# Kernel optimization log

Hardware: AMD Instinct MI355X
Metric: run time of the kernel (lower is better)

## Reference

```python
import jax, jax.numpy as jnp
import numpy as np

jax.config.update("jax_enable_x64", True)  # window_sum runs cumsums in double, as in the torch source

WIN = 7
EPS = 0.01


def _gradient(I):
    # forward finite differences, cropping to [D-1, H-1, W-1] (same=False path, reduction='mean')
    c = I[:, :, 1:, 1:, 1:]
    dx = c - I[:, :, :-1, 1:, 1:]
    dy = c - I[:, :, 1:, :-1, 1:]
    dz = c - I[:, :, 1:, 1:, :-1]
    return dx, dy, dz


def _window_sum(I, win):
    # 3D box-filter via triple cumsum on a zero-padded double-precision volume
    if win == 1:
        return I
    half = win // 2
    pad = (half + win % 2, half)
    Ip = jnp.pad(I, ((0, 0), (0, 0), pad, pad, pad)).astype(jnp.float64)
    cs = jnp.cumsum(jnp.cumsum(jnp.cumsum(Ip, axis=2), axis=3), axis=4)
    x, y, z = I.shape[2:]
    w = win
    out = (cs[:, :, w:, w:, w:] - cs[:, :, w:, w:, :z] - cs[:, :, w:, :y, w:]
           - cs[:, :, :x, w:, w:] + cs[:, :, w:, :y, :z] + cs[:, :, :x, w:, :z]
           + cs[:, :, :x, :y, w:] - cs[:, :, :x, :y, :z])
    return out.astype(jnp.float32)


def setup_inputs() -> dict:
    key = jax.random.key(0)
    k1, k2 = jax.random.split(key)
    shape = (2, 1, 160, 192, 160)
    Ii = jax.random.normal(k1, shape, dtype=jnp.float32)
    Ji = jax.random.normal(k2, shape, dtype=jnp.float32)
    return {"Ii": Ii, "Ji": Ji}


def reference(Ii, Ji):
    def det(dx, dy, dz):
        return dx * dx + dy * dy + dz * dz + EPS

    dxI, dyI, dzI = _gradient(Ii)
    dxJ, dyJ, dzJ = _gradient(Ji)
    dx_I = _window_sum(dxI, WIN)
    dy_I = _window_sum(dyI, WIN)
    dz_I = _window_sum(dzI, WIN)
    dx_J = _window_sum(dxJ, WIN)
    dy_J = _window_sum(dyJ, WIN)
    dz_J = _window_sum(dzJ, WIN)
    cross = jnp.abs(dx_I * dx_J + dy_I * dy_J + dz_I * dz_J) + EPS
    norm = jnp.sqrt(det(dx_I, dy_I, dz_I) * det(dx_J, dy_J, dz_J))
    return jnp.mean(cross / norm)
```

## Files before the change

### kernel.cpp

```cpp
#include <hip/hip_runtime.h>

#define IYD 192
#define IZD 160
#define PLANE 30720
#define VOLSZ 4915200
#define YG 191
#define ZG 159

#define RAW_V 660
#define RAW_R 44
#define ZB 1320
#define DB 2400
#define ZD_V 540
#define ZD_R 36
#define TB 3480
#define WB 3992
#define LDSF 4504

#define NVOX_INV (1.0f / 9657342.0f)

__global__ __launch_bounds__(256, 4) void grad_sim_tele(
    const float* __restrict__ Ii, const float* __restrict__ Ji,
    float* __restrict__ out)
{
    __shared__ __align__(16) float lds[LDSF];
    const int tid = threadIdx.x;
    const int z0 = (int)blockIdx.x * 32;
    const int y0 = (int)blockIdx.y * 8;
    const int seg = blockIdx.z & 7;
    const int bat = blockIdx.z >> 3;
    const int s0 = seg * 20;
    const int a0 = (seg == 0) ? 0 : (s0 - 3);
    const int aLast = (seg == 7) ? 159 : (s0 + 23);

    const float* __restrict__ bI = Ii + (size_t)bat * VOLSZ;
    const float* __restrict__ bJ = Ji + (size_t)bat * VOLSZ;

    const float* gp[5];
    int lof[5];
    bool okl[5];
#pragma unroll
    for (int k = 0; k < 5; ++k) {
        int idx = tid + 256 * k;
        bool inr = idx < 1170;
        int id2 = inr ? idx : 0;
        int v = id2 / 585;
        int r = id2 - v * 585;
        int yy = r / 39;
        int zz = r - yy * 39;
        int iy = y0 - 3 + yy;
        int iz = z0 - 3 + zz;
        okl[k] = inr && ((unsigned)iy < IYD) && ((unsigned)iz < IZD);
        int iyc = min(max(iy, 0), IYD - 1);
        int izc = min(max(iz, 0), IZD - 1);
        gp[k] = (v ? bJ : bI) + (iyc * IZD + izc);
        lof[k] = inr ? (v * RAW_V + yy * RAW_R + zz) : 43;
    }

    const int zv = tid / 60;
    const int zrr = tid - 60 * zv;
    const int zr = zrr >> 2;
    const int zq = zrr & 3;
    const bool doZ = tid < 120;
    const bool zlo = (z0 == 0) && (zq == 0);
    const bool zhi = (z0 == 128) && (zq == 3);
    const int rawRd = zv * RAW_V + zr * RAW_R + 8 * zq;
    const int zdWr = zv * ZD_V + zr * ZD_R + 8 * zq;

    const bool doY = tid < 128;
    const int yf = tid >> 5;
    const int yv = yf & 1;
    const int yisW = yf >> 1;
    const int ybase = (yisW ? DB : ZB) + yv * ZD_V + (tid & 31);
    const int yout = (yisW ? WB : TB) + yv * 256 + (tid & 31);

    const int oy = tid >> 5;
    const int oz = tid & 31;
    const int ygl = y0 + oy;
    const int vmax = min(3, 190 - ygl);
    const int vmin = max(-3, -ygl);
    const int relHi = oy + vmax + 4;
    const int relLo = oy + vmin + 3;
    const int vHiI = ZB + relHi * ZD_R + oz;
    const int vLoI = ZB + relLo * ZD_R + oz;
    const bool okyz = (ygl < YG) && ((z0 + oz) < ZG);

    float Tr[2][8], Vr[2][8], Wr[2][8], Sdy[2], Sdz[2];
#pragma unroll
    for (int v = 0; v < 2; ++v) {
#pragma unroll
        for (int j = 0; j < 8; ++j) { Tr[v][j] = 0.f; Vr[v][j] = 0.f; Wr[v][j] = 0.f; }
        Sdy[v] = 0.f; Sdz[v] = 0.f;
    }
    float acc = 0.f;

    {
        const int pb = a0 * PLANE;
        float t[5];
#pragma unroll
        for (int k = 0; k < 5; ++k) t[k] = gp[k][pb];
#pragma unroll
        for (int k = 0; k < 5; ++k) lds[lof[k]] = okl[k] ? t[k] : 0.f;
    }
    __syncthreads();

    for (int ag = (a0 & ~7); ag <= aLast; ag += 8) {
#pragma unroll
        for (int p = 0; p < 8; ++p) {
            const int a = ag + p;
            if (a < a0 || a > aLast) continue;

            const bool dof = (a + 1) <= aLast;
            float pf[5];
            if (dof) {
                const int pb = (a + 1) * PLANE;
#pragma unroll
                for (int k = 0; k < 5; ++k) pf[k] = gp[k][pb];
            }
            if (doZ) {
                float C[16];
                const float4* rb = (const float4*)&lds[rawRd];
#pragma unroll
                for (int u = 0; u < 4; ++u) ((float4*)C)[u] = rb[u];
                float D[8];
#pragma unroll
                for (int i = 0; i < 8; ++i) D[i] = C[i + 7] - C[i];
                if (zlo) { D[0] = C[7] - C[3]; D[1] = C[8] - C[3]; D[2] = C[9] - C[3]; }
                if (zhi) { D[4] = C[10] - C[4]; D[5] = C[10] - C[5];
                           D[6] = C[10] - C[6]; D[7] = C[10] - C[7]; }
                if (zlo) { C[1] = 0.f; C[2] = 0.f; C[3] = 0.f; }
                if (zhi) { C[11] = 0.f; C[12] = 0.f; C[13] = 0.f; C[14] = 0.f; }
                float Z[8];
                float w = C[1] + C[2] + C[3] + C[4] + C[5] + C[6] + C[7];
                Z[0] = w;
#pragma unroll
                for (int m = 1; m < 8; ++m) { w += C[m + 7] - C[m]; Z[m] = w; }
                float4* zb = (float4*)&lds[ZB + zdWr];
                zb[0] = make_float4(Z[0], Z[1], Z[2], Z[3]);
                zb[1] = make_float4(Z[4], Z[5], Z[6], Z[7]);
                float4* db = (float4*)&lds[DB + zdWr];
                db[0] = make_float4(D[0], D[1], D[2], D[3]);
                db[1] = make_float4(D[4], D[5], D[6], D[7]);
            }
            __syncthreads();

            if (doY) {
                float h[15];
#pragma unroll
                for (int r = 1; r < 15; ++r) h[r] = lds[ybase + r * ZD_R];
                if (y0 == 0)   { h[1] = 0.f; h[2] = 0.f; h[3] = 0.f; }
                if (y0 == 184) { h[11] = 0.f; h[12] = 0.f; h[13] = 0.f; h[14] = 0.f; }
                float w = h[1] + h[2] + h[3] + h[4] + h[5] + h[6] + h[7];
                lds[yout] = w;
#pragma unroll
                for (int q = 1; q < 8; ++q) {
                    w += h[q + 7] - h[q];
                    lds[yout + q * 32] = w;
                }
            }
            __syncthreads();

            {
                float tI = lds[TB + tid];
                float tJ = lds[TB + 256 + tid];
                float wI = lds[WB + tid];
                float wJ = lds[WB + 256 + tid];
                float vI = lds[vHiI] - lds[vLoI];
                float vJ = lds[vHiI + ZD_V] - lds[vLoI + ZD_V];
                if (a == a0) { vI = 0.f; vJ = 0.f; wI = 0.f; wJ = 0.f; }
                const int p1 = (p + 1) & 7;
                float hdxI = tI - Tr[0][p1];
                float hdxJ = tJ - Tr[1][p1];
                Sdy[0] += vI - Vr[0][p1]; Vr[0][p] = vI;
                Sdy[1] += vJ - Vr[1][p1]; Vr[1][p] = vJ;
                Sdz[0] += wI - Wr[0][p1]; Wr[0][p] = wI;
                Sdz[1] += wJ - Wr[1][p1]; Wr[1][p] = wJ;
                Tr[0][p] = tI; Tr[1][p] = tJ;
                if (p == 0) {
                    if (a == 0) {
                        Tr[0][5] = tI; Tr[0][6] = tI; Tr[0][7] = tI;
                        Tr[1][5] = tJ; Tr[1][6] = tJ; Tr[1][7] = tJ;
                    }
                }
                if (a >= s0 + 4) {
                    float cross = fabsf(hdxI * hdxJ + Sdy[0] * Sdy[1] + Sdz[0] * Sdz[1]) + 0.01f;
                    float dI = hdxI * hdxI + Sdy[0] * Sdy[0] + Sdz[0] * Sdz[0] + 0.01f;
                    float dJ = hdxJ * hdxJ + Sdy[1] * Sdy[1] + Sdz[1] * Sdz[1] + 0.01f;
                    float val = cross * rsqrtf(dI * dJ);
                    if (okyz) acc += val;
                }
            }
            if (dof) {
#pragma unroll
                for (int k = 0; k < 5; ++k) lds[lof[k]] = okl[k] ? pf[k] : 0.f;
            }
            __syncthreads();
        }
    }

    if (seg == 7) {
#pragma unroll
        for (int t = 0; t < 3; ++t) {
            const int sl = t + 1;
            float hdxI = Tr[0][7] - Tr[0][sl];
            float hdxJ = Tr[1][7] - Tr[1][sl];
            Sdy[0] -= Vr[0][sl]; Sdy[1] -= Vr[1][sl];
            Sdz[0] -= Wr[0][sl]; Sdz[1] -= Wr[1][sl];
            float cross = fabsf(hdxI * hdxJ + Sdy[0] * Sdy[1] + Sdz[0] * Sdz[1]) + 0.01f;
            float dI = hdxI * hdxI + Sdy[0] * Sdy[0] + Sdz[0] * Sdz[0] + 0.01f;
            float dJ = hdxJ * hdxJ + Sdy[1] * Sdy[1] + Sdz[1] * Sdz[1] + 0.01f;
            float val = cross * rsqrtf(dI * dJ);
            if (okyz) acc += val;
        }
    }

#pragma unroll
    for (int off = 32; off > 0; off >>= 1) acc += __shfl_down(acc, off, 64);
    __syncthreads();
    if ((tid & 63) == 0) lds[tid >> 6] = acc;
    __syncthreads();
    if (tid == 0)
        atomicAdd(out, (lds[0] + lds[1] + lds[2] + lds[3]) * NVOX_INV);
}

extern "C" void kernel_launch(void* const* d_in, const int* in_sizes, int n_in,
                              void* d_out, int out_size, void* d_ws, size_t ws_size,
                              hipStream_t stream) {
    const float* Ii = (const float*)d_in[0];
    const float* Ji = (const float*)d_in[1];
    float* out = (float*)d_out;
    hipMemsetAsync(d_out, 0, sizeof(float) * (out_size > 0 ? out_size : 1), stream);
    dim3 grid(5, 24, 16);
    grad_sim_tele<<<grid, dim3(256), 0, stream>>>(Ii, Ji, out);
}
```

Before: 86.21 us.

## Software-pipeline z/y/x stages across planes with double-buffered LDS, one barrier per plane

The per-plane z-pass, y-pass and final x-accumulate stages are skewed across consecutive planes, so each stage works on a different plane in the same iteration. LDS buffers are double-buffered by parity, which cuts the barriers per plane from three to one. The dy window difference is also precomputed by the otherwise idle upper 128 threads into a new LDS buffer. LDS use roughly doubles to about 40KB, which may lower occupancy below the four blocks per CU requested, and two extra drain iterations are added per segment.

```diff
diff --git a/kernel.cpp b/kernel.cpp
--- a/kernel.cpp
+++ b/kernel.cpp
@@ -7,19 +7,23 @@
 #define YG 191
 #define ZG 159
 
-#define RAW_V 660
-#define RAW_R 44
-#define ZB 1320
-#define DB 2400
-#define ZD_V 540
-#define ZD_R 36
-#define TB 3480
-#define WB 3992
-#define LDSF 4504
+#define RAWP 1320
+#define RAWV 660
+#define RAWR 44
+#define ZBB 2640
+#define DBB 4800
+#define ZDP 1080
+#define ZDV 540
+#define ZDR 36
+#define TBB 6960
+#define WBB 7984
+#define VBB 9008
+#define SOP 512
+#define LDSF 10032
 
 #define NVOX_INV (1.0f / 9657342.0f)
 
-__global__ __launch_bounds__(256, 4) void grad_sim_tele(
+__global__ __launch_bounds__(256, 4) void grad_sim_pipe(
     const float* __restrict__ Ii, const float* __restrict__ Ji,
     float* __restrict__ out)
 {
@@ -32,6 +36,7 @@
     const int s0 = seg * 20;
     const int a0 = (seg == 0) ? 0 : (s0 - 3);
     const int aLast = (seg == 7) ? 159 : (s0 + 23);
+    const int tEnd = aLast + 2;
 
     const float* __restrict__ bI = Ii + (size_t)bat * VOLSZ;
     const float* __restrict__ bJ = Ji + (size_t)bat * VOLSZ;
@@ -54,7 +59,7 @@
         int iyc = min(max(iy, 0), IYD - 1);
         int izc = min(max(iz, 0), IZD - 1);
         gp[k] = (v ? bJ : bI) + (iyc * IZD + izc);
-        lof[k] = inr ? (v * RAW_V + yy * RAW_R + zz) : 43;
+        lof[k] = inr ? (v * RAWV + yy * RAWR + zz) : 43;
     }
 
     const int zv = tid / 60;
@@ -64,26 +69,33 @@
     const bool doZ = tid < 120;
     const bool zlo = (z0 == 0) && (zq == 0);
     const bool zhi = (z0 == 128) && (zq == 3);
-    const int rawRd = zv * RAW_V + zr * RAW_R + 8 * zq;
-    const int zdWr = zv * ZD_V + zr * ZD_R + 8 * zq;
-
-    const bool doY = tid < 128;
+    const int rawRd = zv * RAWV + zr * RAWR + 8 * zq;
+    const int zdWr = zv * ZDV + zr * ZDR + 8 * zq;
+
     const int yf = tid >> 5;
     const int yv = yf & 1;
     const int yisW = yf >> 1;
-    const int ybase = (yisW ? DB : ZB) + yv * ZD_V + (tid & 31);
-    const int yout = (yisW ? WB : TB) + yv * 256 + (tid & 31);
+    const int ybase0 = (yisW ? DBB : ZBB) + yv * ZDV + (tid & 31);
+    const int yout0 = (yisW ? WBB : TBB) + yv * 256 + (tid & 31);
+
+    const int qv = (tid - 128) & 127;
+    const int voz = qv & 31;
+    const int vvv = (qv >> 6) & 1;
+    const int oyb = (qv >> 5) & 1;
+    int rH36[4], rL36[4], vbo[4];
+#pragma unroll
+    for (int k = 0; k < 4; ++k) {
+        int oyk = oyb + 2 * k;
+        int ygl = y0 + oyk;
+        rH36[k] = (oyk + min(3, 190 - ygl) + 4) * ZDR;
+        rL36[k] = (oyk + max(-3, -ygl) + 3) * ZDR;
+        vbo[k] = vvv * 256 + oyk * 32 + voz;
+    }
+    const int zb2base = vvv * ZDV + voz;
 
     const int oy = tid >> 5;
     const int oz = tid & 31;
-    const int ygl = y0 + oy;
-    const int vmax = min(3, 190 - ygl);
-    const int vmin = max(-3, -ygl);
-    const int relHi = oy + vmax + 4;
-    const int relLo = oy + vmin + 3;
-    const int vHiI = ZB + relHi * ZD_R + oz;
-    const int vLoI = ZB + relLo * ZD_R + oz;
-    const bool okyz = (ygl < YG) && ((z0 + oz) < ZG);
+    const bool okyz = ((y0 + oy) < YG) && ((z0 + oz) < ZG);
 
     float Tr[2][8], Vr[2][8], Wr[2][8], Sdy[2], Sdz[2];
 #pragma unroll
@@ -96,32 +108,37 @@
 
     {
         const int pb = a0 * PLANE;
+        const int po = (a0 & 1) * RAWP;
         float t[5];
 #pragma unroll
         for (int k = 0; k < 5; ++k) t[k] = gp[k][pb];
 #pragma unroll
-        for (int k = 0; k < 5; ++k) lds[lof[k]] = okl[k] ? t[k] : 0.f;
+        for (int k = 0; k < 5; ++k) lds[po + lof[k]] = okl[k] ? t[k] : 0.f;
     }
     __syncthreads();
 
-    for (int ag = (a0 & ~7); ag <= aLast; ag += 8) {
-#pragma unroll
-        for (int p = 0; p < 8; ++p) {
-            const int a = ag + p;
-            if (a < a0 || a > aLast) continue;
-
-            const bool dof = (a + 1) <= aLast;
+    for (int ag = (a0 & ~7); ag <= tEnd; ag += 8) {
+#pragma unroll
+        for (int u = 0; u < 8; ++u) {
+            const int t = ag + u;
+            if (t < a0 || t > tEnd) continue;
+
+            const int par1 = u & 1;
+            const int par2 = (u + 1) & 1;
+
+            const bool dof = (t + 1) <= aLast;
             float pf[5];
             if (dof) {
-                const int pb = (a + 1) * PLANE;
+                const int pb = (t + 1) * PLANE;
 #pragma unroll
                 for (int k = 0; k < 5; ++k) pf[k] = gp[k][pb];
             }
-            if (doZ) {
+
+            if (t <= aLast && doZ) {
                 float C[16];
-                const float4* rb = (const float4*)&lds[rawRd];
-#pragma unroll
-                for (int u = 0; u < 4; ++u) ((float4*)C)[u] = rb[u];
+                const float4* rb = (const float4*)&lds[par1 * RAWP + rawRd];
+#pragma unroll
+                for (int q = 0; q < 4; ++q) ((float4*)C)[q] = rb[q];
                 float D[8];
 #pragma unroll
                 for (int i = 0; i < 8; ++i) D[i] = C[i + 7] - C[i];
@@ -135,39 +152,53 @@
                 Z[0] = w;
 #pragma unroll
                 for (int m = 1; m < 8; ++m) { w += C[m + 7] - C[m]; Z[m] = w; }
-                float4* zb = (float4*)&lds[ZB + zdWr];
+                float4* zb = (float4*)&lds[ZBB + par1 * ZDP + zdWr];
                 zb[0] = make_float4(Z[0], Z[1], Z[2], Z[3]);
                 zb[1] = make_float4(Z[4], Z[5], Z[6], Z[7]);
-                float4* db = (float4*)&lds[DB + zdWr];
+                float4* db = (float4*)&lds[DBB + par1 * ZDP + zdWr];
                 db[0] = make_float4(D[0], D[1], D[2], D[3]);
                 db[1] = make_float4(D[4], D[5], D[6], D[7]);
             }
-            __syncthreads();
-
-            if (doY) {
-                float h[15];
-#pragma unroll
-                for (int r = 1; r < 15; ++r) h[r] = lds[ybase + r * ZD_R];
-                if (y0 == 0)   { h[1] = 0.f; h[2] = 0.f; h[3] = 0.f; }
-                if (y0 == 184) { h[11] = 0.f; h[12] = 0.f; h[13] = 0.f; h[14] = 0.f; }
-                float w = h[1] + h[2] + h[3] + h[4] + h[5] + h[6] + h[7];
-                lds[yout] = w;
-#pragma unroll
-                for (int q = 1; q < 8; ++q) {
-                    w += h[q + 7] - h[q];
-                    lds[yout + q * 32] = w;
+
+            if (t - 1 >= a0 && t - 1 <= aLast) {
+                if (tid < 128) {
+                    const int ybase = ybase0 + par2 * ZDP;
+                    const int yout = yout0 + par2 * SOP;
+                    float h[15];
+#pragma unroll
+                    for (int r = 1; r < 15; ++r) h[r] = lds[ybase + r * ZDR];
+                    if (y0 == 0)   { h[1] = 0.f; h[2] = 0.f; h[3] = 0.f; }
+                    if (y0 == 184) { h[11] = 0.f; h[12] = 0.f; h[13] = 0.f; h[14] = 0.f; }
+                    float w = h[1] + h[2] + h[3] + h[4] + h[5] + h[6] + h[7];
+                    lds[yout] = w;
+#pragma unroll
+                    for (int q = 1; q < 8; ++q) {
+                        w += h[q + 7] - h[q];
+                        lds[yout + q * 32] = w;
+                    }
+                } else {
+                    const int zb2 = ZBB + par2 * ZDP + zb2base;
+                    const int vout = VBB + par2 * SOP;
+#pragma unroll
+                    for (int k = 0; k < 4; ++k) {
+                        float hi = lds[zb2 + rH36[k]];
+                        float lo = lds[zb2 + rL36[k]];
+                        lds[vout + vbo[k]] = hi - lo;
+                    }
                 }
             }
-            __syncthreads();
-
-            {
-                float tI = lds[TB + tid];
-                float tJ = lds[TB + 256 + tid];
-                float wI = lds[WB + tid];
-                float wJ = lds[WB + 256 + tid];
-                float vI = lds[vHiI] - lds[vLoI];
-                float vJ = lds[vHiI + ZD_V] - lds[vLoI + ZD_V];
+
+            if (t - 2 >= a0) {
+                const int a = t - 2;
+                const int sb = par1 * SOP;
+                float tI = lds[TBB + sb + tid];
+                float tJ = lds[TBB + sb + 256 + tid];
+                float wI = lds[WBB + sb + tid];
+                float wJ = lds[WBB + sb + 256 + tid];
+                float vI = lds[VBB + sb + tid];
+                float vJ = lds[VBB + sb + 256 + tid];
                 if (a == a0) { vI = 0.f; vJ = 0.f; wI = 0.f; wJ = 0.f; }
+                const int p = (u + 6) & 7;
                 const int p1 = (p + 1) & 7;
                 float hdxI = tI - Tr[0][p1];
                 float hdxJ = tJ - Tr[1][p1];
@@ -176,11 +207,9 @@
                 Sdz[0] += wI - Wr[0][p1]; Wr[0][p] = wI;
                 Sdz[1] += wJ - Wr[1][p1]; Wr[1][p] = wJ;
                 Tr[0][p] = tI; Tr[1][p] = tJ;
-                if (p == 0) {
-                    if (a == 0) {
-                        Tr[0][5] = tI; Tr[0][6] = tI; Tr[0][7] = tI;
-                        Tr[1][5] = tJ; Tr[1][6] = tJ; Tr[1][7] = tJ;
-                    }
+                if (p == 0 && a == 0) {
+                    Tr[0][5] = tI; Tr[0][6] = tI; Tr[0][7] = tI;
+                    Tr[1][5] = tJ; Tr[1][6] = tJ; Tr[1][7] = tJ;
                 }
                 if (a >= s0 + 4) {
                     float cross = fabsf(hdxI * hdxJ + Sdy[0] * Sdy[1] + Sdz[0] * Sdz[1]) + 0.01f;
@@ -190,9 +219,11 @@
                     if (okyz) acc += val;
                 }
             }
+
             if (dof) {
-#pragma unroll
-                for (int k = 0; k < 5; ++k) lds[lof[k]] = okl[k] ? pf[k] : 0.f;
+                const int po = ((u + 1) & 1) * RAWP;
+#pragma unroll
+                for (int k = 0; k < 5; ++k) lds[po + lof[k]] = okl[k] ? pf[k] : 0.f;
             }
             __syncthreads();
         }
@@ -200,8 +231,8 @@
 
     if (seg == 7) {
 #pragma unroll
-        for (int t = 0; t < 3; ++t) {
-            const int sl = t + 1;
+        for (int tt = 0; tt < 3; ++tt) {
+            const int sl = tt + 1;
             float hdxI = Tr[0][7] - Tr[0][sl];
             float hdxJ = Tr[1][7] - Tr[1][sl];
             Sdy[0] -= Vr[0][sl]; Sdy[1] -= Vr[1][sl];
@@ -231,5 +262,5 @@
     float* out = (float*)d_out;
     hipMemsetAsync(d_out, 0, sizeof(float) * (out_size > 0 ? out_size : 1), stream);
     dim3 grid(5, 24, 16);
-    grad_sim_tele<<<grid, dim3(256), 0, stream>>>(Ii, Ji, out);
+    grad_sim_pipe<<<grid, dim3(256), 0, stream>>>(Ii, Ji, out);
 }
```

Measured after the change: 90.87 us. 5.4% more time.

## Vectorize plane loads to float4, widen Y-pass, halve depth segments

Applied to the files above, without the earlier changes.

Each input plane tile is now loaded as float4 chunks aligned to 4-element z boundaries, replacing scalar gathers. The raw LDS layout shifts by one element to suit this. The Y-direction box sum now runs on 64 threads, each handling a float4 of z and half of the y outputs. The x-axis is split into 4 segments of 40 instead of 8 of 20, which cuts halo recomputation but halves the grid to 960 blocks, lowering parallelism. Out-of-range chunks are zeroed by multiplying with a mask, which assumes the clamped loads hold finite values.

```diff
diff --git a/kernel.cpp b/kernel.cpp
--- a/kernel.cpp
+++ b/kernel.cpp
@@ -7,19 +7,19 @@
 #define YG 191
 #define ZG 159
 
-#define RAW_V 660
-#define RAW_R 44
-#define ZB 1320
-#define DB 2400
-#define ZD_V 540
-#define ZD_R 36
-#define TB 3480
-#define WB 3992
-#define LDSF 4504
+#define RAWV 660
+#define RAWR 44
+#define ZBB 1324
+#define DBB 2404
+#define ZDV 540
+#define ZDR 36
+#define TBB 3484
+#define WBB 3996
+#define LDSF 4508
 
 #define NVOX_INV (1.0f / 9657342.0f)
 
-__global__ __launch_bounds__(256, 4) void grad_sim_tele(
+__global__ __launch_bounds__(256, 4) void grad_sim_v7(
     const float* __restrict__ Ii, const float* __restrict__ Ji,
     float* __restrict__ out)
 {
@@ -27,34 +27,48 @@
     const int tid = threadIdx.x;
     const int z0 = (int)blockIdx.x * 32;
     const int y0 = (int)blockIdx.y * 8;
-    const int seg = blockIdx.z & 7;
-    const int bat = blockIdx.z >> 3;
-    const int s0 = seg * 20;
+    const int seg = blockIdx.z & 3;
+    const int bat = blockIdx.z >> 2;
+    const int s0 = seg * 40;
     const int a0 = (seg == 0) ? 0 : (s0 - 3);
-    const int aLast = (seg == 7) ? 159 : (s0 + 23);
+    const int aLast = (seg == 3) ? 159 : (s0 + 43);
 
     const float* __restrict__ bI = Ii + (size_t)bat * VOLSZ;
     const float* __restrict__ bJ = Ji + (size_t)bat * VOLSZ;
 
-    const float* gp[5];
-    int lof[5];
-    bool okl[5];
-#pragma unroll
-    for (int k = 0; k < 5; ++k) {
-        int idx = tid + 256 * k;
-        bool inr = idx < 1170;
-        int id2 = inr ? idx : 0;
-        int v = id2 / 585;
-        int r = id2 - v * 585;
-        int yy = r / 39;
-        int zz = r - yy * 39;
-        int iy = y0 - 3 + yy;
-        int iz = z0 - 3 + zz;
-        okl[k] = inr && ((unsigned)iy < IYD) && ((unsigned)iz < IZD);
+    const float* gq0;
+    const float* gq1;
+    int lq0, lq1;
+    float mq0, mq1;
+    {
+        int q = tid;
+        int v = q / 150;
+        int rr = q - v * 150;
+        int row = rr / 10;
+        int qd = rr - row * 10;
+        int iy = y0 - 3 + row;
+        int izb = z0 - 4 + 4 * qd;
+        bool ok = ((unsigned)iy < IYD) && (izb >= 0) && (izb + 3 <= 159);
         int iyc = min(max(iy, 0), IYD - 1);
-        int izc = min(max(iz, 0), IZD - 1);
-        gp[k] = (v ? bJ : bI) + (iyc * IZD + izc);
-        lof[k] = inr ? (v * RAW_V + yy * RAW_R + zz) : 43;
+        int izc = min(max(izb, 0), 156);
+        gq0 = (v ? bJ : bI) + (iyc * IZD + izc);
+        lq0 = v * RAWV + row * RAWR + 4 * qd;
+        mq0 = ok ? 1.f : 0.f;
+    }
+    {
+        int q = 256 + tid;
+        int v = q / 150;
+        int rr = q - v * 150;
+        int row = rr / 10;
+        int qd = rr - row * 10;
+        int iy = y0 - 3 + row;
+        int izb = z0 - 4 + 4 * qd;
+        bool ok = ((unsigned)iy < IYD) && (izb >= 0) && (izb + 3 <= 159);
+        int iyc = min(max(iy, 0), IYD - 1);
+        int izc = min(max(izb, 0), 156);
+        gq1 = (v ? bJ : bI) + (iyc * IZD + izc);
+        lq1 = v * RAWV + row * RAWR + 4 * qd;
+        mq1 = ok ? 1.f : 0.f;
     }
 
     const int zv = tid / 60;
@@ -64,25 +78,27 @@
     const bool doZ = tid < 120;
     const bool zlo = (z0 == 0) && (zq == 0);
     const bool zhi = (z0 == 128) && (zq == 3);
-    const int rawRd = zv * RAW_V + zr * RAW_R + 8 * zq;
-    const int zdWr = zv * ZD_V + zr * ZD_R + 8 * zq;
-
-    const bool doY = tid < 128;
-    const int yf = tid >> 5;
-    const int yv = yf & 1;
-    const int yisW = yf >> 1;
-    const int ybase = (yisW ? DB : ZB) + yv * ZD_V + (tid & 31);
-    const int yout = (yisW ? WB : TB) + yv * 256 + (tid & 31);
+    const int rawRd = zv * RAWV + zr * RAWR + 8 * zq;
+    const int zdWr = zv * ZDV + zr * ZDR + 8 * zq;
+
+    const int e2half = tid & 1;
+    const int e2c = tid >> 1;
+    const int e2zq = e2c & 7;
+    const int e2f = (e2c >> 3) & 1;
+    const int e2v = e2c >> 4;
+    const bool doY = tid < 64;
+    const int e2base = (e2f ? DBB : ZBB) + e2v * ZDV + 4 * e2zq;
+    const int e2out = (e2f ? WBB : TBB) + e2v * 256 + 4 * e2zq;
+    const float mlo = (y0 == 0) ? 0.f : 1.f;
+    const float mhi = (y0 == 184) ? 0.f : 1.f;
 
     const int oy = tid >> 5;
     const int oz = tid & 31;
     const int ygl = y0 + oy;
     const int vmax = min(3, 190 - ygl);
     const int vmin = max(-3, -ygl);
-    const int relHi = oy + vmax + 4;
-    const int relLo = oy + vmin + 3;
-    const int vHiI = ZB + relHi * ZD_R + oz;
-    const int vLoI = ZB + relLo * ZD_R + oz;
+    const int vHiI = ZBB + (oy + vmax + 4) * ZDR + oz;
+    const int vLoI = ZBB + (oy + vmin + 3) * ZDR + oz;
     const bool okyz = (ygl < YG) && ((z0 + oz) < ZG);
 
     float Tr[2][8], Vr[2][8], Wr[2][8], Sdy[2], Sdz[2];
@@ -95,80 +111,116 @@
     float acc = 0.f;
 
     {
-        const int pb = a0 * PLANE;
-        float t[5];
-#pragma unroll
-        for (int k = 0; k < 5; ++k) t[k] = gp[k][pb];
-#pragma unroll
-        for (int k = 0; k < 5; ++k) lds[lof[k]] = okl[k] ? t[k] : 0.f;
+        const size_t pb = (size_t)a0 * PLANE;
+        float4 t0 = *(const float4*)(gq0 + pb);
+        t0.x *= mq0; t0.y *= mq0; t0.z *= mq0; t0.w *= mq0;
+        *(float4*)&lds[lq0] = t0;
+        if (tid < 44) {
+            float4 t1 = *(const float4*)(gq1 + pb);
+            t1.x *= mq1; t1.y *= mq1; t1.z *= mq1; t1.w *= mq1;
+            *(float4*)&lds[lq1] = t1;
+        }
     }
     __syncthreads();
 
     for (int ag = (a0 & ~7); ag <= aLast; ag += 8) {
 #pragma unroll
-        for (int p = 0; p < 8; ++p) {
-            const int a = ag + p;
+        for (int u = 0; u < 8; ++u) {
+            const int a = ag + u;
             if (a < a0 || a > aLast) continue;
 
             const bool dof = (a + 1) <= aLast;
-            float pf[5];
+            float4 pf0, pf1;
             if (dof) {
-                const int pb = (a + 1) * PLANE;
-#pragma unroll
-                for (int k = 0; k < 5; ++k) pf[k] = gp[k][pb];
-            }
+                const size_t pb = (size_t)(a + 1) * PLANE;
+                pf0 = *(const float4*)(gq0 + pb);
+                if (tid < 44) pf1 = *(const float4*)(gq1 + pb);
+            }
+
             if (doZ) {
                 float C[16];
                 const float4* rb = (const float4*)&lds[rawRd];
 #pragma unroll
-                for (int u = 0; u < 4; ++u) ((float4*)C)[u] = rb[u];
+                for (int q = 0; q < 4; ++q) ((float4*)C)[q] = rb[q];
                 float D[8];
 #pragma unroll
-                for (int i = 0; i < 8; ++i) D[i] = C[i + 7] - C[i];
-                if (zlo) { D[0] = C[7] - C[3]; D[1] = C[8] - C[3]; D[2] = C[9] - C[3]; }
-                if (zhi) { D[4] = C[10] - C[4]; D[5] = C[10] - C[5];
-                           D[6] = C[10] - C[6]; D[7] = C[10] - C[7]; }
-                if (zlo) { C[1] = 0.f; C[2] = 0.f; C[3] = 0.f; }
-                if (zhi) { C[11] = 0.f; C[12] = 0.f; C[13] = 0.f; C[14] = 0.f; }
+                for (int i = 0; i < 8; ++i) D[i] = C[i + 8] - C[i + 1];
+                if (zlo) { D[0] = C[8] - C[4]; D[1] = C[9] - C[4]; D[2] = C[10] - C[4]; }
+                if (zhi) { D[4] = C[11] - C[5]; D[5] = C[11] - C[6];
+                           D[6] = C[11] - C[7]; D[7] = C[11] - C[8]; }
+                if (zlo) { C[2] = 0.f; C[3] = 0.f; C[4] = 0.f; }
                 float Z[8];
-                float w = C[1] + C[2] + C[3] + C[4] + C[5] + C[6] + C[7];
+                float w = C[2] + C[3] + C[4] + C[5] + C[6] + C[7] + C[8];
                 Z[0] = w;
 #pragma unroll
-                for (int m = 1; m < 8; ++m) { w += C[m + 7] - C[m]; Z[m] = w; }
-                float4* zb = (float4*)&lds[ZB + zdWr];
+                for (int m = 1; m < 8; ++m) { w += C[m + 8] - C[m + 1]; Z[m] = w; }
+                float4* zb = (float4*)&lds[ZBB + zdWr];
                 zb[0] = make_float4(Z[0], Z[1], Z[2], Z[3]);
                 zb[1] = make_float4(Z[4], Z[5], Z[6], Z[7]);
-                float4* db = (float4*)&lds[DB + zdWr];
+                float4* db = (float4*)&lds[DBB + zdWr];
                 db[0] = make_float4(D[0], D[1], D[2], D[3]);
                 db[1] = make_float4(D[4], D[5], D[6], D[7]);
             }
             __syncthreads();
 
             if (doY) {
-                float h[15];
-#pragma unroll
-                for (int r = 1; r < 15; ++r) h[r] = lds[ybase + r * ZD_R];
-                if (y0 == 0)   { h[1] = 0.f; h[2] = 0.f; h[3] = 0.f; }
-                if (y0 == 184) { h[11] = 0.f; h[12] = 0.f; h[13] = 0.f; h[14] = 0.f; }
-                float w = h[1] + h[2] + h[3] + h[4] + h[5] + h[6] + h[7];
-                lds[yout] = w;
-#pragma unroll
-                for (int q = 1; q < 8; ++q) {
-                    w += h[q + 7] - h[q];
-                    lds[yout + q * 32] = w;
+                float4 r[11];
+                const int r0 = e2half ? 4 : 1;
+#pragma unroll
+                for (int i = 0; i < 11; ++i)
+                    r[i] = *(const float4*)&lds[e2base + (r0 + i) * ZDR];
+                if (e2half == 0) {
+                    r[0].x *= mlo; r[0].y *= mlo; r[0].z *= mlo; r[0].w *= mlo;
+                    r[1].x *= mlo; r[1].y *= mlo; r[1].z *= mlo; r[1].w *= mlo;
+                    r[2].x *= mlo; r[2].y *= mlo; r[2].z *= mlo; r[2].w *= mlo;
+                    r[10].x *= mhi; r[10].y *= mhi; r[10].z *= mhi; r[10].w *= mhi;
+                    float4 w;
+                    w.x = r[0].x + r[1].x + r[2].x + r[3].x + r[4].x + r[5].x + r[6].x;
+                    w.y = r[0].y + r[1].y + r[2].y + r[3].y + r[4].y + r[5].y + r[6].y;
+                    w.z = r[0].z + r[1].z + r[2].z + r[3].z + r[4].z + r[5].z + r[6].z;
+                    w.w = r[0].w + r[1].w + r[2].w + r[3].w + r[4].w + r[5].w + r[6].w;
+                    *(float4*)&lds[e2out] = w;
+#pragma unroll
+                    for (int m = 1; m < 4; ++m) {
+                        w.x += r[m + 6].x - r[m - 1].x;
+                        w.y += r[m + 6].y - r[m - 1].y;
+                        w.z += r[m + 6].z - r[m - 1].z;
+                        w.w += r[m + 6].w - r[m - 1].w;
+                        *(float4*)&lds[e2out + m * 32] = w;
+                    }
+                } else {
+                    r[7].x *= mhi; r[7].y *= mhi; r[7].z *= mhi; r[7].w *= mhi;
+                    r[8].x *= mhi; r[8].y *= mhi; r[8].z *= mhi; r[8].w *= mhi;
+                    r[9].x *= mhi; r[9].y *= mhi; r[9].z *= mhi; r[9].w *= mhi;
+                    r[10].x *= mhi; r[10].y *= mhi; r[10].z *= mhi; r[10].w *= mhi;
+                    float4 w;
+                    w.x = r[1].x + r[2].x + r[3].x + r[4].x + r[5].x + r[6].x + r[7].x;
+                    w.y = r[1].y + r[2].y + r[3].y + r[4].y + r[5].y + r[6].y + r[7].y;
+                    w.z = r[1].z + r[2].z + r[3].z + r[4].z + r[5].z + r[6].z + r[7].z;
+                    w.w = r[1].w + r[2].w + r[3].w + r[4].w + r[5].w + r[6].w + r[7].w;
+                    *(float4*)&lds[e2out + 4 * 32] = w;
+#pragma unroll
+                    for (int m = 1; m < 4; ++m) {
+                        w.x += r[m + 7].x - r[m].x;
+                        w.y += r[m + 7].y - r[m].y;
+                        w.z += r[m + 7].z - r[m].z;
+                        w.w += r[m + 7].w - r[m].w;
+                        *(float4*)&lds[e2out + (4 + m) * 32] = w;
+                    }
                 }
             }
             __syncthreads();
 
             {
-                float tI = lds[TB + tid];
-                float tJ = lds[TB + 256 + tid];
-                float wI = lds[WB + tid];
-                float wJ = lds[WB + 256 + tid];
+                float tI = lds[TBB + tid];
+                float tJ = lds[TBB + 256 + tid];
+                float wI = lds[WBB + tid];
+                float wJ = lds[WBB + 256 + tid];
                 float vI = lds[vHiI] - lds[vLoI];
-                float vJ = lds[vHiI + ZD_V] - lds[vLoI + ZD_V];
+                float vJ = lds[vHiI + ZDV] - lds[vLoI + ZDV];
                 if (a == a0) { vI = 0.f; vJ = 0.f; wI = 0.f; wJ = 0.f; }
-                const int p1 = (p + 1) & 7;
+                const int p = u;
+                const int p1 = (u + 1) & 7;
                 float hdxI = tI - Tr[0][p1];
                 float hdxJ = tJ - Tr[1][p1];
                 Sdy[0] += vI - Vr[0][p1]; Vr[0][p] = vI;
@@ -176,11 +228,9 @@
                 Sdz[0] += wI - Wr[0][p1]; Wr[0][p] = wI;
                 Sdz[1] += wJ - Wr[1][p1]; Wr[1][p] = wJ;
                 Tr[0][p] = tI; Tr[1][p] = tJ;
-                if (p == 0) {
-                    if (a == 0) {
-                        Tr[0][5] = tI; Tr[0][6] = tI; Tr[0][7] = tI;
-                        Tr[1][5] = tJ; Tr[1][6] = tJ; Tr[1][7] = tJ;
-                    }
+                if (p == 0 && a == 0) {
+                    Tr[0][5] = tI; Tr[0][6] = tI; Tr[0][7] = tI;
+                    Tr[1][5] = tJ; Tr[1][6] = tJ; Tr[1][7] = tJ;
                 }
                 if (a >= s0 + 4) {
                     float cross = fabsf(hdxI * hdxJ + Sdy[0] * Sdy[1] + Sdz[0] * Sdz[1]) + 0.01f;
@@ -190,18 +240,23 @@
                     if (okyz) acc += val;
                 }
             }
+
             if (dof) {
-#pragma unroll
-                for (int k = 0; k < 5; ++k) lds[lof[k]] = okl[k] ? pf[k] : 0.f;
+                pf0.x *= mq0; pf0.y *= mq0; pf0.z *= mq0; pf0.w *= mq0;
+                *(float4*)&lds[lq0] = pf0;
+                if (tid < 44) {
+                    pf1.x *= mq1; pf1.y *= mq1; pf1.z *= mq1; pf1.w *= mq1;
+                    *(float4*)&lds[lq1] = pf1;
+                }
             }
             __syncthreads();
         }
     }
 
-    if (seg == 7) {
-#pragma unroll
-        for (int t = 0; t < 3; ++t) {
-            const int sl = t + 1;
+    if (seg == 3) {
+#pragma unroll
+        for (int tt = 0; tt < 3; ++tt) {
+            const int sl = tt + 1;
             float hdxI = Tr[0][7] - Tr[0][sl];
             float hdxJ = Tr[1][7] - Tr[1][sl];
             Sdy[0] -= Vr[0][sl]; Sdy[1] -= Vr[1][sl];
@@ -230,6 +285,6 @@
     const float* Ji = (const float*)d_in[1];
     float* out = (float*)d_out;
     hipMemsetAsync(d_out, 0, sizeof(float) * (out_size > 0 ? out_size : 1), stream);
-    dim3 grid(5, 24, 16);
-    grad_sim_tele<<<grid, dim3(256), 0, stream>>>(Ii, Ji, out);
+    dim3 grid(5, 24, 8);
+    grad_sim_v7<<<grid, dim3(256), 0, stream>>>(Ii, Ji, out);
 }
```

After: 77.73 us. -9.8%, faster.

## Double-buffer per-plane stage buffers, vectorize raw loads, and cut barriers per plane

Applied to the files above, without the earlier changes.

The per-plane pipeline moves from three barriers to two by double-buffering the intermediate window-sum buffers. The final accumulation stage now reads the previous plane's results while the current plane's z and y sums are produced. Global loads become float4 with a multiplicative mask, and the y-direction box sum is vectorized over float4 columns. The z-derived sums are now computed from windowed differences of z and y sums rather than a separate difference buffer. Costs are a larger LDS footprint and more complex indexing and boundary handling, which could harm occupancy or correctness at the edges.

```diff
diff --git a/kernel.cpp b/kernel.cpp
--- a/kernel.cpp
+++ b/kernel.cpp
@@ -7,19 +7,33 @@
 #define YG 191
 #define ZG 159
 
-#define RAW_V 660
-#define RAW_R 44
-#define ZB 1320
-#define DB 2400
-#define ZD_V 540
-#define ZD_R 36
-#define TB 3480
-#define WB 3992
-#define LDSF 4504
+#define RAWV 660
+#define RAWR 44
+#define PB0 1320
+#define PBS 2360
+#define ZBV 540
+#define ZBR 36
+#define YBO 1080
+#define YBV 352
+#define YBR 44
+#define TBO 1784
+#define TBV 288
+#define TBR 36
+#define LDSF 6040
 
 #define NVOX_INV (1.0f / 9657342.0f)
 
-__global__ __launch_bounds__(256, 4) void grad_sim_tele(
+__device__ __forceinline__ float4 f4add(float4 a, float4 b) {
+    return make_float4(a.x + b.x, a.y + b.y, a.z + b.z, a.w + b.w);
+}
+__device__ __forceinline__ float4 f4sub(float4 a, float4 b) {
+    return make_float4(a.x - b.x, a.y - b.y, a.z - b.z, a.w - b.w);
+}
+__device__ __forceinline__ float4 f4scale(float4 a, float s) {
+    return make_float4(a.x * s, a.y * s, a.z * s, a.w * s);
+}
+
+__global__ __launch_bounds__(256, 4) void grad_sim_v8(
     const float* __restrict__ Ii, const float* __restrict__ Ji,
     float* __restrict__ out)
 {
@@ -36,25 +50,29 @@
     const float* __restrict__ bI = Ii + (size_t)bat * VOLSZ;
     const float* __restrict__ bJ = Ji + (size_t)bat * VOLSZ;
 
-    const float* gp[5];
-    int lof[5];
-    bool okl[5];
-#pragma unroll
-    for (int k = 0; k < 5; ++k) {
-        int idx = tid + 256 * k;
-        bool inr = idx < 1170;
-        int id2 = inr ? idx : 0;
-        int v = id2 / 585;
-        int r = id2 - v * 585;
-        int yy = r / 39;
-        int zz = r - yy * 39;
-        int iy = y0 - 3 + yy;
-        int iz = z0 - 3 + zz;
-        okl[k] = inr && ((unsigned)iy < IYD) && ((unsigned)iz < IZD);
-        int iyc = min(max(iy, 0), IYD - 1);
-        int izc = min(max(iz, 0), IZD - 1);
-        gp[k] = (v ? bJ : bI) + (iyc * IZD + izc);
-        lof[k] = inr ? (v * RAW_V + yy * RAW_R + zz) : 43;
+    const float* gq0; const float* gq1;
+    int lq0, lq1; float mq0, mq1;
+    {
+        int q = tid;
+        int v = q / 150; int rr = q - v * 150;
+        int row = rr / 10; int qd = rr - row * 10;
+        int iy = y0 - 3 + row; int izb = z0 - 4 + 4 * qd;
+        bool ok = ((unsigned)iy < IYD) && (izb >= 0) && (izb + 3 <= 159);
+        int iyc = min(max(iy, 0), IYD - 1); int izc = min(max(izb, 0), 156);
+        gq0 = (v ? bJ : bI) + (iyc * IZD + izc);
+        lq0 = v * RAWV + row * RAWR + 4 * qd;
+        mq0 = ok ? 1.f : 0.f;
+    }
+    {
+        int q = 256 + tid;
+        int v = q / 150; int rr = q - v * 150;
+        int row = rr / 10; int qd = rr - row * 10;
+        int iy = y0 - 3 + row; int izb = z0 - 4 + 4 * qd;
+        bool ok = ((unsigned)iy < IYD) && (izb >= 0) && (izb + 3 <= 159);
+        int iyc = min(max(iy, 0), IYD - 1); int izc = min(max(izb, 0), 156);
+        gq1 = (v ? bJ : bI) + (iyc * IZD + izc);
+        lq1 = v * RAWV + row * RAWR + 4 * qd;
+        mq1 = ok ? 1.f : 0.f;
     }
 
     const int zv = tid / 60;
@@ -62,27 +80,41 @@
     const int zr = zrr >> 2;
     const int zq = zrr & 3;
     const bool doZ = tid < 120;
-    const bool zlo = (z0 == 0) && (zq == 0);
-    const bool zhi = (z0 == 128) && (zq == 3);
-    const int rawRd = zv * RAW_V + zr * RAW_R + 8 * zq;
-    const int zdWr = zv * ZD_V + zr * ZD_R + 8 * zq;
-
-    const bool doY = tid < 128;
-    const int yf = tid >> 5;
-    const int yv = yf & 1;
-    const int yisW = yf >> 1;
-    const int ybase = (yisW ? DB : ZB) + yv * ZD_V + (tid & 31);
-    const int yout = (yisW ? WB : TB) + yv * 256 + (tid & 31);
+    const bool zlo1 = (z0 == 0) && (zq == 0);
+    const int rawRd = zv * RAWV + zr * RAWR + 8 * zq;
+    const int zbWr = zv * ZBV + zr * ZBR + 8 * zq;
+
+    const int t2a = tid - 128;
+    const bool doYA = (t2a >= 0) && (t2a < 20);
+    const int t2s = doYA ? t2a : 0;
+    const int aZq = t2s % 10;
+    const int aV = t2s / 10;
+    const int aRawB = aV * RAWV + 4 * aZq;
+    const int aYbB = YBO + aV * YBV + 4 * aZq;
+    const float mlo = (y0 == 0) ? 0.f : 1.f;
+    const float mhi = (y0 == 184) ? 0.f : 1.f;
+
+    const bool doTB = tid < 64;
+    const int bV = tid >> 5;
+    const int bR = tid & 31;
+    const int bOy = bR >> 2;
+    const int bZq = bR & 3;
+    const bool zlo2 = (z0 == 0) && (bZq == 0);
+    const int ybRd = YBO + bV * YBV + bOy * YBR + 8 * bZq;
+    const int tbWr = TBO + bV * TBV + bOy * TBR + 8 * bZq;
 
     const int oy = tid >> 5;
     const int oz = tid & 31;
     const int ygl = y0 + oy;
     const int vmax = min(3, 190 - ygl);
     const int vmin = max(-3, -ygl);
-    const int relHi = oy + vmax + 4;
-    const int relLo = oy + vmin + 3;
-    const int vHiI = ZB + relHi * ZD_R + oz;
-    const int vLoI = ZB + relLo * ZD_R + oz;
+    const int oT = TBO + oy * TBR + oz;
+    const int oVhi = (oy + vmax + 4) * ZBR + oz;
+    const int oVlo = (oy + vmin + 3) * ZBR + oz;
+    const int relHiZ = min(oz + 8, (z0 == 128) ? 35 : 63);
+    const int relLoZ = max(oz + 1, (z0 == 0) ? 4 : 0);
+    const int oWhi = YBO + oy * YBR + relHiZ;
+    const int oWlo = YBO + oy * YBR + relLoZ;
     const bool okyz = (ygl < YG) && ((z0 + oz) < ZG);
 
     float Tr[2][8], Vr[2][8], Wr[2][8], Sdy[2], Sdz[2];
@@ -95,79 +127,94 @@
     float acc = 0.f;
 
     {
-        const int pb = a0 * PLANE;
-        float t[5];
-#pragma unroll
-        for (int k = 0; k < 5; ++k) t[k] = gp[k][pb];
-#pragma unroll
-        for (int k = 0; k < 5; ++k) lds[lof[k]] = okl[k] ? t[k] : 0.f;
+        const size_t pb = (size_t)a0 * PLANE;
+        float4 t0 = f4scale(*(const float4*)(gq0 + pb), mq0);
+        *(float4*)&lds[lq0] = t0;
+        if (tid < 44) {
+            float4 t1 = f4scale(*(const float4*)(gq1 + pb), mq1);
+            *(float4*)&lds[lq1] = t1;
+        }
     }
     __syncthreads();
 
-    for (int ag = (a0 & ~7); ag <= aLast; ag += 8) {
-#pragma unroll
-        for (int p = 0; p < 8; ++p) {
-            const int a = ag + p;
-            if (a < a0 || a > aLast) continue;
-
-            const bool dof = (a + 1) <= aLast;
-            float pf[5];
+    for (int ag = (a0 & ~7); ag <= aLast + 1; ag += 8) {
+#pragma unroll
+        for (int u = 0; u < 8; ++u) {
+            const int t = ag + u;
+            if (t < a0 || t > aLast + 1) continue;
+            const int PBp = PB0 + (u & 1) * PBS;
+            const int PBq = PB0 + ((u + 1) & 1) * PBS;
+
+            const bool dof = (t + 1) <= aLast;
+            float4 pf0, pf1;
             if (dof) {
-                const int pb = (a + 1) * PLANE;
-#pragma unroll
-                for (int k = 0; k < 5; ++k) pf[k] = gp[k][pb];
-            }
-            if (doZ) {
+                const size_t pb = (size_t)(t + 1) * PLANE;
+                pf0 = *(const float4*)(gq0 + pb);
+                if (tid < 44) pf1 = *(const float4*)(gq1 + pb);
+            }
+
+            if (t <= aLast && doZ) {
                 float C[16];
                 const float4* rb = (const float4*)&lds[rawRd];
 #pragma unroll
-                for (int u = 0; u < 4; ++u) ((float4*)C)[u] = rb[u];
-                float D[8];
-#pragma unroll
-                for (int i = 0; i < 8; ++i) D[i] = C[i + 7] - C[i];
-                if (zlo) { D[0] = C[7] - C[3]; D[1] = C[8] - C[3]; D[2] = C[9] - C[3]; }
-                if (zhi) { D[4] = C[10] - C[4]; D[5] = C[10] - C[5];
-                           D[6] = C[10] - C[6]; D[7] = C[10] - C[7]; }
-                if (zlo) { C[1] = 0.f; C[2] = 0.f; C[3] = 0.f; }
-                if (zhi) { C[11] = 0.f; C[12] = 0.f; C[13] = 0.f; C[14] = 0.f; }
+                for (int q = 0; q < 4; ++q) ((float4*)C)[q] = rb[q];
+                if (zlo1) { C[2] = 0.f; C[3] = 0.f; C[4] = 0.f; }
                 float Z[8];
-                float w = C[1] + C[2] + C[3] + C[4] + C[5] + C[6] + C[7];
+                float w = C[2] + C[3] + C[4] + C[5] + C[6] + C[7] + C[8];
                 Z[0] = w;
 #pragma unroll
-                for (int m = 1; m < 8; ++m) { w += C[m + 7] - C[m]; Z[m] = w; }
-                float4* zb = (float4*)&lds[ZB + zdWr];
+                for (int m = 1; m < 8; ++m) { w += C[m + 8] - C[m + 1]; Z[m] = w; }
+                float4* zb = (float4*)&lds[PBp + zbWr];
                 zb[0] = make_float4(Z[0], Z[1], Z[2], Z[3]);
                 zb[1] = make_float4(Z[4], Z[5], Z[6], Z[7]);
-                float4* db = (float4*)&lds[DB + zdWr];
-                db[0] = make_float4(D[0], D[1], D[2], D[3]);
-                db[1] = make_float4(D[4], D[5], D[6], D[7]);
-            }
-            __syncthreads();
-
-            if (doY) {
-                float h[15];
-#pragma unroll
-                for (int r = 1; r < 15; ++r) h[r] = lds[ybase + r * ZD_R];
-                if (y0 == 0)   { h[1] = 0.f; h[2] = 0.f; h[3] = 0.f; }
-                if (y0 == 184) { h[11] = 0.f; h[12] = 0.f; h[13] = 0.f; h[14] = 0.f; }
-                float w = h[1] + h[2] + h[3] + h[4] + h[5] + h[6] + h[7];
-                lds[yout] = w;
-#pragma unroll
-                for (int q = 1; q < 8; ++q) {
-                    w += h[q + 7] - h[q];
-                    lds[yout + q * 32] = w;
-                }
-            }
-            __syncthreads();
-
-            {
-                float tI = lds[TB + tid];
-                float tJ = lds[TB + 256 + tid];
-                float wI = lds[WB + tid];
-                float wJ = lds[WB + 256 + tid];
-                float vI = lds[vHiI] - lds[vLoI];
-                float vJ = lds[vHiI + ZD_V] - lds[vLoI + ZD_V];
-                if (a == a0) { vI = 0.f; vJ = 0.f; wI = 0.f; wJ = 0.f; }
+            }
+
+            if (t <= aLast && doYA) {
+                const float* rb = &lds[aRawB];
+                float4 r1 = f4scale(*(const float4*)&rb[1 * RAWR], mlo);
+                float4 r2 = f4scale(*(const float4*)&rb[2 * RAWR], mlo);
+                float4 r3 = f4scale(*(const float4*)&rb[3 * RAWR], mlo);
+                float4 r4 = *(const float4*)&rb[4 * RAWR];
+                float4 r5 = *(const float4*)&rb[5 * RAWR];
+                float4 r6 = *(const float4*)&rb[6 * RAWR];
+                float4 r7 = *(const float4*)&rb[7 * RAWR];
+                float4 w = f4add(f4add(f4add(r1, r2), f4add(r3, r4)),
+                                 f4add(f4add(r5, r6), r7));
+                *(float4*)&lds[PBp + aYbB] = w;
+                float4 rn;
+                rn = *(const float4*)&rb[8 * RAWR];
+                w = f4add(w, f4sub(rn, r1));
+                *(float4*)&lds[PBp + aYbB + 1 * YBR] = w;
+                rn = *(const float4*)&rb[9 * RAWR];
+                w = f4add(w, f4sub(rn, r2));
+                *(float4*)&lds[PBp + aYbB + 2 * YBR] = w;
+                rn = *(const float4*)&rb[10 * RAWR];
+                w = f4add(w, f4sub(rn, r3));
+                *(float4*)&lds[PBp + aYbB + 3 * YBR] = w;
+                rn = f4scale(*(const float4*)&rb[11 * RAWR], mhi);
+                w = f4add(w, f4sub(rn, r4));
+                *(float4*)&lds[PBp + aYbB + 4 * YBR] = w;
+                rn = f4scale(*(const float4*)&rb[12 * RAWR], mhi);
+                w = f4add(w, f4sub(rn, r5));
+                *(float4*)&lds[PBp + aYbB + 5 * YBR] = w;
+                rn = f4scale(*(const float4*)&rb[13 * RAWR], mhi);
+                w = f4add(w, f4sub(rn, r6));
+                *(float4*)&lds[PBp + aYbB + 6 * YBR] = w;
+                rn = f4scale(*(const float4*)&rb[14 * RAWR], mhi);
+                w = f4add(w, f4sub(rn, r7));
+                *(float4*)&lds[PBp + aYbB + 7 * YBR] = w;
+            }
+
+            if (t - 1 >= a0) {
+                const int aa = t - 1;
+                float tI = lds[PBq + oT];
+                float tJ = lds[PBq + oT + TBV];
+                float vI = lds[PBq + oVhi] - lds[PBq + oVlo];
+                float vJ = lds[PBq + oVhi + ZBV] - lds[PBq + oVlo + ZBV];
+                float wI = lds[PBq + oWhi] - lds[PBq + oWlo];
+                float wJ = lds[PBq + oWhi + YBV] - lds[PBq + oWlo + YBV];
+                if (aa == a0) { vI = 0.f; vJ = 0.f; wI = 0.f; wJ = 0.f; }
+                const int p = (u + 7) & 7;
                 const int p1 = (p + 1) & 7;
                 float hdxI = tI - Tr[0][p1];
                 float hdxJ = tJ - Tr[1][p1];
@@ -176,13 +223,11 @@
                 Sdz[0] += wI - Wr[0][p1]; Wr[0][p] = wI;
                 Sdz[1] += wJ - Wr[1][p1]; Wr[1][p] = wJ;
                 Tr[0][p] = tI; Tr[1][p] = tJ;
-                if (p == 0) {
-                    if (a == 0) {
-                        Tr[0][5] = tI; Tr[0][6] = tI; Tr[0][7] = tI;
-                        Tr[1][5] = tJ; Tr[1][6] = tJ; Tr[1][7] = tJ;
-                    }
+                if (p == 0 && aa == 0) {
+                    Tr[0][5] = tI; Tr[0][6] = tI; Tr[0][7] = tI;
+                    Tr[1][5] = tJ; Tr[1][6] = tJ; Tr[1][7] = tJ;
                 }
-                if (a >= s0 + 4) {
+                if (aa >= s0 + 4) {
                     float cross = fabsf(hdxI * hdxJ + Sdy[0] * Sdy[1] + Sdz[0] * Sdz[1]) + 0.01f;
                     float dI = hdxI * hdxI + Sdy[0] * Sdy[0] + Sdz[0] * Sdz[0] + 0.01f;
                     float dJ = hdxJ * hdxJ + Sdy[1] * Sdy[1] + Sdz[1] * Sdz[1] + 0.01f;
@@ -190,9 +235,26 @@
                     if (okyz) acc += val;
                 }
             }
+            __syncthreads();
+
+            if (t <= aLast && doTB) {
+                float C[16];
+                const float4* yb = (const float4*)&lds[PBp + ybRd];
+#pragma unroll
+                for (int q = 0; q < 4; ++q) ((float4*)C)[q] = yb[q];
+                if (zlo2) { C[2] = 0.f; C[3] = 0.f; C[4] = 0.f; }
+                float Z[8];
+                float w = C[2] + C[3] + C[4] + C[5] + C[6] + C[7] + C[8];
+                Z[0] = w;
+#pragma unroll
+                for (int m = 1; m < 8; ++m) { w += C[m + 8] - C[m + 1]; Z[m] = w; }
+                float4* tb = (float4*)&lds[PBp + tbWr];
+                tb[0] = make_float4(Z[0], Z[1], Z[2], Z[3]);
+                tb[1] = make_float4(Z[4], Z[5], Z[6], Z[7]);
+            }
             if (dof) {
-#pragma unroll
-                for (int k = 0; k < 5; ++k) lds[lof[k]] = okl[k] ? pf[k] : 0.f;
+                *(float4*)&lds[lq0] = f4scale(pf0, mq0);
+                if (tid < 44) *(float4*)&lds[lq1] = f4scale(pf1, mq1);
             }
             __syncthreads();
         }
@@ -200,8 +262,8 @@
 
     if (seg == 7) {
 #pragma unroll
-        for (int t = 0; t < 3; ++t) {
-            const int sl = t + 1;
+        for (int tt = 0; tt < 3; ++tt) {
+            const int sl = tt + 1;
             float hdxI = Tr[0][7] - Tr[0][sl];
             float hdxJ = Tr[1][7] - Tr[1][sl];
             Sdy[0] -= Vr[0][sl]; Sdy[1] -= Vr[1][sl];
@@ -231,5 +293,5 @@
     float* out = (float*)d_out;
     hipMemsetAsync(d_out, 0, sizeof(float) * (out_size > 0 ? out_size : 1), stream);
     dim3 grid(5, 24, 16);
-    grad_sim_tele<<<grid, dim3(256), 0, stream>>>(Ii, Ji, out);
-}
+    grad_sim_v8<<<grid, dim3(256), 0, stream>>>(Ii, Ji, out);
+}
```

Result: slower. 95.33 us (+10.6%).
